# Optimization experiments

Hardware: AMD Instinct MI355X
Metric: run time of the kernel (lower is better)

## Reference

```python
import jax, jax.numpy as jnp
import numpy as np

# Standard SMPL kinematic tree (child -> parent); root's entry unused.
PARENTS = np.array([0, 0, 0, 0, 1, 2, 3, 4, 5, 6, 7, 8, 9, 9, 9, 12, 13, 14, 16, 17, 18, 19, 20, 21], dtype=np.int32)
N_JOINTS = 24


def _rodrigues(r):
    # r: [..., 3] axis-angle -> [..., 3, 3] rotation matrices.
    # Original adds N(0,1e-8) noise to avoid div-by-zero; we use a deterministic eps.
    theta = jnp.linalg.norm(r, axis=-1, keepdims=True) + 1e-8
    rh = r / theta
    cos = jnp.cos(theta)[..., None]
    sin = jnp.sin(theta)[..., None]
    z = jnp.zeros_like(rh[..., 0])
    K = jnp.stack([z, -rh[..., 2], rh[..., 1],
                   rh[..., 2], z, -rh[..., 0],
                   -rh[..., 1], rh[..., 0], z], axis=-1).reshape(r.shape[:-1] + (3, 3))
    outer = rh[..., :, None] * rh[..., None, :]
    eye = jnp.eye(3, dtype=r.dtype)
    return cos * eye + (1.0 - cos) * outer + sin * K


def setup_inputs() -> dict:
    key = jax.random.key(0)
    ks = jax.random.split(key, 7)
    N, V, J, B = 512, 6890, 24, 10
    beta = jax.random.normal(ks[0], (N, B), dtype=jnp.float32)
    pose = jax.random.normal(ks[1], (N, J * 3), dtype=jnp.float32)
    v_template = jax.random.normal(ks[2], (V, 3), dtype=jnp.float32)
    shapedirs = jax.random.normal(ks[3], (V, 3, B), dtype=jnp.float32) * 0.03
    posedirs = jax.random.normal(ks[4], (V, 3, (J - 1) * 9), dtype=jnp.float32) * 0.01
    J_regressor = jax.random.uniform(ks[5], (J, V), dtype=jnp.float32)
    J_regressor = J_regressor / jnp.sum(J_regressor, axis=1, keepdims=True)  # NonNegUnitSum(axis=1)
    weights = jax.random.uniform(ks[6], (V, J), dtype=jnp.float32)
    weights = weights / jnp.sum(weights, axis=1, keepdims=True)  # NonNegUnitSum(axis=1)
    return {"beta": beta, "pose": pose, "v_template": v_template, "shapedirs": shapedirs,
            "posedirs": posedirs, "J_regressor": J_regressor, "weights": weights}


def reference(beta, pose, v_template, shapedirs, posedirs, J_regressor, weights):
    N = beta.shape[0]
    dt = beta.dtype
    # Shape blendshapes: [N,V,3]
    v_shaped = jnp.einsum('nb,vcb->nvc', beta, shapedirs) + v_template
    # Joint locations: [N,J,3]
    J_loc = jnp.einsum('jv,nvc->njc', J_regressor, v_shaped)
    # Per-joint rotations: [N,24,3,3]
    R = _rodrigues(pose.reshape(N, N_JOINTS, 3))
    # Pose blendshapes
    lrotmin = (R[:, 1:] - jnp.eye(3, dtype=dt)).reshape(N, (N_JOINTS - 1) * 9)
    v_posed = v_shaped + jnp.einsum('np,vcp->nvc', lrotmin, posedirs)
    # Kinematic chain of 4x4 transforms
    bottom = jnp.broadcast_to(jnp.array([0.0, 0.0, 0.0, 1.0], dtype=dt), (N, 1, 4))

    def make_T(Rm, t):  # [N,3,3], [N,3] -> [N,4,4]
        return jnp.concatenate([jnp.concatenate([Rm, t[..., None]], axis=-1), bottom], axis=-2)

    G = [make_T(R[:, 0], J_loc[:, 0])]
    for i in range(1, N_JOINTS):
        p = int(PARENTS[i])
        G.append(jnp.matmul(G[p], make_T(R[:, i], J_loc[:, i] - J_loc[:, p])))
    G = jnp.stack(G, axis=1)  # [N,24,4,4]
    # Remove rest-pose joint translation: G[...,:,3] -= G @ [J,0]
    Jh = jnp.concatenate([J_loc, jnp.zeros_like(J_loc[..., :1])], axis=-1)  # [N,24,4]
    RJ = jnp.einsum('njab,njb->nja', G, Jh)
    G = G - jnp.pad(RJ[..., None], ((0, 0), (0, 0), (0, 0), (3, 0)))
    # Linear blend skinning: per-vertex blended transform [N,V,4,4]
    T = jnp.einsum('njab,vj->nvab', G, weights)
    vh = jnp.concatenate([v_posed, jnp.ones_like(v_posed[..., :1])], axis=-1)  # [N,V,4]
    v = jnp.einsum('nvab,nvb->nva', T, vh)
    return v[..., :3]
```

## Files before the change

### kernel.cpp

```cpp
#include <hip/hip_runtime.h>

#define V_CNT 6890
#define N_B 512
#define NP 207
#define KPAD 224
#define RTOT 20670
#define RPAD 20736
#define PREP_BLKS 2268
#define JS1_BLKS 192
#define W_BLKS 27
#define FUSE_X 108
#define FUSE_BLKS 864

typedef unsigned short ushort_t;
typedef __attribute__((ext_vector_type(4))) float f32x4;
typedef __attribute__((ext_vector_type(8))) short s16x8;
typedef __attribute__((ext_vector_type(4))) short s16x4;

#define O_PART 0u
#define O_G2   65536u
#define O_A    655360u
#define O_W    917504u
#define O_B    1441792u

__device__ __constant__ int PAR[24] = {0,0,0,0,1,2,3,4,5,6,7,8,9,9,9,12,13,14,16,17,18,19,20,21};
__device__ __constant__ int LVL[36] = {
    1, 2, 3,-1,   4, 5, 6,-1,   7, 8, 9,-1,
   10,11,12,13,  14,-1,-1,-1,  15,16,17,-1,
   18,19,-1,-1,  20,21,-1,-1,  22,23,-1,-1};

__device__ __forceinline__ ushort_t f2bf(float f) {
    union { float f; unsigned u; } x; x.f = f;
    unsigned u = x.u + 0x7fffu + ((x.u >> 16) & 1u);
    return (ushort_t)(u >> 16);
}
__device__ __forceinline__ float bf2f(ushort_t h) {
    union { unsigned u; float f; } x; x.u = ((unsigned)h) << 16;
    return x.f;
}

__global__ __launch_bounds__(256) void k_pre(const float* __restrict__ pdirs,
                                             const float* __restrict__ sdirs,
                                             const float* __restrict__ vtemp,
                                             const float* __restrict__ jreg,
                                             const float* __restrict__ wts,
                                             ushort_t* __restrict__ Bswz,
                                             float* __restrict__ part,
                                             ushort_t* __restrict__ Wp) {
    int b = blockIdx.x;
    int tid = threadIdx.x;
    if (b < PREP_BLKS) {
        int g = b * 256 + tid;
        int rtile = g / 448;
        int rem = g - rtile * 448;
        int kc = rem >> 6;
        int lane = rem & 63;
        int quad = lane >> 4, lm = lane & 15;
        int r = rtile * 16 + lm;
        int k0 = kc * 32 + quad * 8;
        s16x8 pk;
        if (r < RTOT) {
            const float* pr = pdirs + (size_t)r * NP;
            const float* sr = sdirs + (size_t)r * 10;
#pragma unroll
            for (int i = 0; i < 8; i++) {
                int k = k0 + i;
                float v = 0.f;
                if (k < NP) v = pr[k];
                else if (k < 217) v = sr[k - NP];
                pk[i] = (short)f2bf(v);
            }
        } else {
#pragma unroll
            for (int i = 0; i < 8; i++) pk[i] = 0;
        }
        *(s16x8*)(Bswz + (size_t)g * 8) = pk;
    } else if (b < PREP_BLKS + JS1_BLKS) {
        int b2 = b - PREP_BLKS;
        int ch = b2 & 7;
        int j = b2 >> 3;
        int v0 = ch * 862;
        int vend = v0 + 862; if (vend > V_CNT) vend = V_CNT;
        float acc[33];
#pragma unroll
        for (int i = 0; i < 33; i++) acc[i] = 0.f;
        for (int v = v0 + tid; v < vend; v += 256) {
            float r = jreg[j * V_CNT + v];
            const float* sd = sdirs + v * 30;
#pragma unroll
            for (int i = 0; i < 30; i++) acc[i] += r * sd[i];
            acc[30] += r * vtemp[v * 3 + 0];
            acc[31] += r * vtemp[v * 3 + 1];
            acc[32] += r * vtemp[v * 3 + 2];
        }
#pragma unroll
        for (int off = 32; off > 0; off >>= 1) {
#pragma unroll
            for (int i = 0; i < 33; i++) acc[i] += __shfl_down(acc[i], off);
        }
        __shared__ float red[4][33];
        int w = tid >> 6, lane = tid & 63;
        if (lane == 0) {
#pragma unroll
            for (int i = 0; i < 33; i++) red[w][i] = acc[i];
        }
        __syncthreads();
        if (tid < 33) {
            float s = red[0][tid] + red[1][tid] + red[2][tid] + red[3][tid];
            part[b2 * 33 + tid] = s;
        }
    } else {
        int v = (b - PREP_BLKS - JS1_BLKS) * 256 + tid;
        ushort_t o[32];
        if (v < V_CNT) {
            const float* wr = wts + v * 24;
#pragma unroll
            for (int j = 0; j < 24; j++) o[j] = f2bf(wr[j]);
        } else {
#pragma unroll
            for (int j = 0; j < 24; j++) o[j] = 0;
        }
#pragma unroll
        for (int j = 24; j < 32; j++) o[j] = 0;
#pragma unroll
        for (int q = 0; q < 4; q++)
            *(s16x8*)(Wp + (size_t)v * 32 + q * 8) = *(s16x8*)&o[q * 8];
    }
}

__global__ __launch_bounds__(128) void k_chain(const float* __restrict__ beta,
                                               const float* __restrict__ pose,
                                               const float* __restrict__ part,
                                               ushort_t* __restrict__ G2,
                                               ushort_t* __restrict__ Aswz) {
    __shared__ float JSl[720];
    __shared__ float JTl[72];
    __shared__ float Rl[2][24][9];
    __shared__ float Jl[2][24][3];
    __shared__ float Tm[2][24][16];
    __shared__ float G[2][24][16];
    __shared__ float Gp[2][24][12];
    int tid = threadIdx.x;

    for (int t = tid; t < 792; t += 128) {
        int j = t / 33, i = t - j * 33;
        float s = 0.f;
#pragma unroll
        for (int c = 0; c < 8; c++) s += part[(j * 8 + c) * 33 + i];
        if (i < 30) JSl[j * 30 + i] = s;
        else        JTl[j * 3 + (i - 30)] = s;
    }
    __syncthreads();

    int sub = tid >> 6, lane = tid & 63;
    int n = blockIdx.x * 2 + sub;

    if (lane < 24) {
        int t = lane;
        float x = pose[n * 72 + t * 3 + 0];
        float y = pose[n * 72 + t * 3 + 1];
        float z = pose[n * 72 + t * 3 + 2];
        float th = sqrtf(x * x + y * y + z * z) + 1e-8f;
        float inv = 1.f / th;
        float rx = x * inv, ry = y * inv, rz = z * inv;
        float c = cosf(th), s = sinf(th), omc = 1.f - c;
        Rl[sub][t][0] = c + omc * rx * rx;
        Rl[sub][t][1] = omc * rx * ry - s * rz;
        Rl[sub][t][2] = omc * rx * rz + s * ry;
        Rl[sub][t][3] = omc * ry * rx + s * rz;
        Rl[sub][t][4] = c + omc * ry * ry;
        Rl[sub][t][5] = omc * ry * rz - s * rx;
        Rl[sub][t][6] = omc * rz * rx - s * ry;
        Rl[sub][t][7] = omc * rz * ry + s * rx;
        Rl[sub][t][8] = c + omc * rz * rz;
#pragma unroll
        for (int cc = 0; cc < 3; cc++) {
            float a = JTl[t * 3 + cc];
#pragma unroll
            for (int b = 0; b < 10; b++) a += beta[n * 10 + b] * JSl[(t * 3 + cc) * 10 + b];
            Jl[sub][t][cc] = a;
        }
    }
    __syncthreads();
    if (lane < 24) {
        int t = lane;
        int p = PAR[t];
        float tx, ty, tz;
        if (t == 0) { tx = Jl[sub][0][0]; ty = Jl[sub][0][1]; tz = Jl[sub][0][2]; }
        else { tx = Jl[sub][t][0] - Jl[sub][p][0]; ty = Jl[sub][t][1] - Jl[sub][p][1]; tz = Jl[sub][t][2] - Jl[sub][p][2]; }
        Tm[sub][t][0] = Rl[sub][t][0]; Tm[sub][t][1] = Rl[sub][t][1]; Tm[sub][t][2]  = Rl[sub][t][2]; Tm[sub][t][3]  = tx;
        Tm[sub][t][4] = Rl[sub][t][3]; Tm[sub][t][5] = Rl[sub][t][4]; Tm[sub][t][6]  = Rl[sub][t][5]; Tm[sub][t][7]  = ty;
        Tm[sub][t][8] = Rl[sub][t][6]; Tm[sub][t][9] = Rl[sub][t][7]; Tm[sub][t][10] = Rl[sub][t][8]; Tm[sub][t][11] = tz;
        Tm[sub][t][12] = 0.f; Tm[sub][t][13] = 0.f; Tm[sub][t][14] = 0.f; Tm[sub][t][15] = 1.f;
    }
    __syncthreads();
    if (lane < 16) G[sub][0][lane] = Tm[sub][0][lane];
    __syncthreads();
#pragma unroll
    for (int p9 = 0; p9 < 9; p9++) {
        int slot = lane >> 4, el = lane & 15;
        int j = LVL[p9 * 4 + slot];
        if (j >= 0) {
            int par = PAR[j];
            int a = el >> 2, bb = el & 3;
            float s = G[sub][par][a * 4 + 0] * Tm[sub][j][0 * 4 + bb]
                    + G[sub][par][a * 4 + 1] * Tm[sub][j][1 * 4 + bb]
                    + G[sub][par][a * 4 + 2] * Tm[sub][j][2 * 4 + bb]
                    + G[sub][par][a * 4 + 3] * Tm[sub][j][3 * 4 + bb];
            G[sub][j][el] = s;
        }
        __syncthreads();
    }
    if (lane < 24) {
        int t = lane;
        float jx = Jl[sub][t][0], jy = Jl[sub][t][1], jz = Jl[sub][t][2];
#pragma unroll
        for (int a = 0; a < 3; a++) {
            float g0 = G[sub][t][a * 4 + 0], g1 = G[sub][t][a * 4 + 1];
            float g2 = G[sub][t][a * 4 + 2], g3 = G[sub][t][a * 4 + 3];
            Gp[sub][t][a * 4 + 0] = g0;
            Gp[sub][t][a * 4 + 1] = g1;
            Gp[sub][t][a * 4 + 2] = g2;
            Gp[sub][t][a * 4 + 3] = g3 - (g0 * jx + g1 * jy + g2 * jz);
        }
    }
    __syncthreads();
    {
        int quad = lane >> 4, lm = lane & 15;
        s16x8 pk;
#pragma unroll
        for (int jj = 0; jj < 8; jj++) {
            int joint = quad * 8 + jj;
            float val = (joint < 24 && lm < 12) ? Gp[sub][joint][lm] : 0.f;
            pk[jj] = (short)f2bf(val);
        }
        *(s16x8*)(G2 + (size_t)n * 512 + lane * 8) = pk;
    }
    if (lane < 28) {
        int kc = lane >> 2, quad2 = lane & 3;
        s16x8 pk;
#pragma unroll
        for (int j = 0; j < 8; j++) {
            int k = kc * 32 + quad2 * 8 + j;
            float val;
            if (k < NP) {
                int jo = 1 + k / 9;
                int e = k - (jo - 1) * 9;
                float d = (e == 0 || e == 4 || e == 8) ? 1.f : 0.f;
                val = Rl[sub][jo][e] - d;
            } else if (k < 217) {
                val = beta[n * 10 + (k - NP)];
            } else val = 0.f;
            pk[j] = (short)f2bf(val);
        }
        *(s16x8*)(Aswz + (((size_t)(n >> 4) * 7 + kc) * 64 + (quad2 * 16 + (n & 15))) * 8) = pk;
    }
}

__global__ __launch_bounds__(256) void k_fused(const ushort_t* __restrict__ Aswz,
                                               const ushort_t* __restrict__ Bswz,
                                               const ushort_t* __restrict__ Wp,
                                               const ushort_t* __restrict__ G2,
                                               const float* __restrict__ vtemp,
                                               float* __restrict__ out) {
    __shared__ ushort_t vp[4][96][36];
    int bid = blockIdx.x;
    int tt = (bid & 7) * FUSE_X + (bid >> 3);
    int bx = tt >> 3, by = tt & 7;
    int tid = threadIdx.x, w = tid >> 6, lane = tid & 63;
    int quad = lane >> 4, lm = lane & 15;
    int rh = w & 1, nh = w >> 1;
    int n_w = by * 64 + nh * 32;
    int vs_w = bx * 64 + rh * 32;
    int rtile0 = bx * 12 + rh * 6;
    int ntile0 = by * 4 + nh * 2;

    f32x4 acc[2][6];
#pragma unroll
    for (int a = 0; a < 2; a++)
#pragma unroll
        for (int b = 0; b < 6; b++) acc[a][b] = (f32x4)0.f;

    s16x8 af[2][2], bf[2][6];
#pragma unroll
    for (int mt = 0; mt < 2; mt++)
        af[0][mt] = *(const s16x8*)(Aswz + ((size_t)(ntile0 + mt) * 7 + 0) * 512 + lane * 8);
#pragma unroll
    for (int rt = 0; rt < 6; rt++)
        bf[0][rt] = *(const s16x8*)(Bswz + ((size_t)(rtile0 + rt) * 7 + 0) * 512 + lane * 8);
#pragma unroll
    for (int kc = 0; kc < 7; kc++) {
        int cur = kc & 1, nxt = cur ^ 1;
        if (kc < 6) {
#pragma unroll
            for (int mt = 0; mt < 2; mt++)
                af[nxt][mt] = *(const s16x8*)(Aswz + ((size_t)(ntile0 + mt) * 7 + kc + 1) * 512 + lane * 8);
#pragma unroll
            for (int rt = 0; rt < 6; rt++)
                bf[nxt][rt] = *(const s16x8*)(Bswz + ((size_t)(rtile0 + rt) * 7 + kc + 1) * 512 + lane * 8);
        }
#pragma unroll
        for (int mt = 0; mt < 2; mt++)
#pragma unroll
            for (int rt = 0; rt < 6; rt++)
                acc[mt][rt] = __builtin_amdgcn_mfma_f32_16x16x32_bf16(af[cur][mt], bf[cur][rt], acc[mt][rt], 0, 0, 0);
    }

    float vt[6];
#pragma unroll
    for (int rt = 0; rt < 6; rt++) {
        int col = bx * 192 + rh * 96 + rt * 16 + lm;
        vt[rt] = (col < RTOT) ? vtemp[col] : 0.f;
    }
#pragma unroll
    for (int mt = 0; mt < 2; mt++) {
#pragma unroll
        for (int rt = 0; rt < 6; rt++) {
            int rl = rt * 16 + lm;
            int nl0 = mt * 16 + quad * 4;
            s16x4 pk;
            pk[0] = (short)f2bf(acc[mt][rt][0] + vt[rt]);
            pk[1] = (short)f2bf(acc[mt][rt][1] + vt[rt]);
            pk[2] = (short)f2bf(acc[mt][rt][2] + vt[rt]);
            pk[3] = (short)f2bf(acc[mt][rt][3] + vt[rt]);
            *(s16x4*)&vp[w][rl][nl0] = pk;
        }
    }

    s16x8 wf[2];
#pragma unroll
    for (int mt = 0; mt < 2; mt++)
        wf[mt] = *(const s16x8*)(Wp + (size_t)(vs_w + mt * 16 + lm) * 32 + quad * 8);

    s16x8 ga = *(const s16x8*)(G2 + (size_t)n_w * 512 + lane * 8);
    s16x8 gb = *(const s16x8*)(G2 + (size_t)(n_w + 1) * 512 + lane * 8);
#pragma unroll 1
    for (int t = 0; t < 16; t++) {
        int na = n_w + 2 * t;
        s16x8 gan, gbn;
        if (t < 15) {
            gan = *(const s16x8*)(G2 + (size_t)(na + 2) * 512 + lane * 8);
            gbn = *(const s16x8*)(G2 + (size_t)(na + 3) * 512 + lane * 8);
        }
        f32x4 ta[2], tb[2];
#pragma unroll
        for (int mt = 0; mt < 2; mt++) {
            ta[mt] = __builtin_amdgcn_mfma_f32_16x16x32_bf16(ga, wf[mt], (f32x4)0.f, 0, 0, 0);
            tb[mt] = __builtin_amdgcn_mfma_f32_16x16x32_bf16(gb, wf[mt], (f32x4)0.f, 0, 0, 0);
        }
        if (quad < 3) {
#pragma unroll
            for (int mt = 0; mt < 2; mt++) {
                int v = vs_w + mt * 16 + lm;
                if (v < V_CNT) {
                    int vloc = mt * 16 + lm;
                    unsigned pw0 = *(const unsigned*)&vp[w][vloc * 3 + 0][2 * t];
                    unsigned pw1 = *(const unsigned*)&vp[w][vloc * 3 + 1][2 * t];
                    unsigned pw2 = *(const unsigned*)&vp[w][vloc * 3 + 2][2 * t];
                    float p0a = bf2f((ushort_t)(pw0 & 0xffffu)), p0b = bf2f((ushort_t)(pw0 >> 16));
                    float p1a = bf2f((ushort_t)(pw1 & 0xffffu)), p1b = bf2f((ushort_t)(pw1 >> 16));
                    float p2a = bf2f((ushort_t)(pw2 & 0xffffu)), p2b = bf2f((ushort_t)(pw2 >> 16));
                    float oa = ta[mt][3] + ta[mt][0] * p0a + ta[mt][1] * p1a + ta[mt][2] * p2a;
                    float ob = tb[mt][3] + tb[mt][0] * p0b + tb[mt][1] * p1b + tb[mt][2] * p2b;
                    out[((size_t)na * V_CNT + v) * 3 + quad] = oa;
                    out[((size_t)(na + 1) * V_CNT + v) * 3 + quad] = ob;
                }
            }
        }
        ga = gan; gb = gbn;
    }
}

extern "C" void kernel_launch(void* const* d_in, const int* in_sizes, int n_in,
                              void* d_out, int out_size, void* d_ws, size_t ws_size,
                              hipStream_t stream) {
    const float* beta  = (const float*)d_in[0];
    const float* pose  = (const float*)d_in[1];
    const float* vtemp = (const float*)d_in[2];
    const float* sdirs = (const float*)d_in[3];
    const float* pdirs = (const float*)d_in[4];
    const float* jreg  = (const float*)d_in[5];
    const float* wts   = (const float*)d_in[6];
    char* ws = (char*)d_ws;
    float*    ws_part = (float*)(ws + O_PART);
    ushort_t* ws_G2   = (ushort_t*)(ws + O_G2);
    ushort_t* ws_A    = (ushort_t*)(ws + O_A);
    ushort_t* ws_W    = (ushort_t*)(ws + O_W);
    ushort_t* ws_B    = (ushort_t*)(ws + O_B);
    float* out = (float*)d_out;

    k_pre<<<dim3(PREP_BLKS + JS1_BLKS + W_BLKS), dim3(256), 0, stream>>>(
        pdirs, sdirs, vtemp, jreg, wts, ws_B, ws_part, ws_W);
    k_chain<<<dim3(N_B / 2), dim3(128), 0, stream>>>(beta, pose, ws_part, ws_G2, ws_A);
    k_fused<<<dim3(FUSE_BLKS), dim3(256), 0, stream>>>(ws_A, ws_B, ws_W, ws_G2, vtemp, out);
}
```

Baseline: 137.8 us.

## Fuse posedirs and weights bf16 conversion into the main GEMM kernel

Drops the pre-pass that converted posedirs/shapedirs and skinning weights to swizzled bf16 workspace buffers. The fused kernel now reads fp32 posedirs and weights directly and converts them in registers before the MFMA. This removes a full write-then-read round trip of the large posedirs matrix (~17 MB fp32). The cost is that each posedirs element is re-read by every n-tile block, about eight times, in fp32 with unaligned, uncoalesced row-strided loads. The software double-buffering of the K loop is also lost.

```diff
diff --git a/kernel.cpp b/kernel.cpp
--- a/kernel.cpp
+++ b/kernel.cpp
@@ -3,12 +3,8 @@
 #define V_CNT 6890
 #define N_B 512
 #define NP 207
-#define KPAD 224
 #define RTOT 20670
-#define RPAD 20736
-#define PREP_BLKS 2268
 #define JS1_BLKS 192
-#define W_BLKS 27
 #define FUSE_X 108
 #define FUSE_BLKS 864
 
@@ -20,8 +16,6 @@
 #define O_PART 0u
 #define O_G2   65536u
 #define O_A    655360u
-#define O_W    917504u
-#define O_B    1441792u
 
 __device__ __constant__ int PAR[24] = {0,0,0,0,1,2,3,4,5,6,7,8,9,9,9,12,13,14,16,17,18,19,20,21};
 __device__ __constant__ int LVL[36] = {
@@ -38,93 +32,47 @@
     union { unsigned u; float f; } x; x.u = ((unsigned)h) << 16;
     return x.f;
 }
-
-__global__ __launch_bounds__(256) void k_pre(const float* __restrict__ pdirs,
+__device__ __forceinline__ f32x4 ld4u(const float* p) {
+    f32x4 v; __builtin_memcpy(&v, p, 16); return v;
+}
+
+__global__ __launch_bounds__(256) void k_pre(const float* __restrict__ jreg,
                                              const float* __restrict__ sdirs,
                                              const float* __restrict__ vtemp,
-                                             const float* __restrict__ jreg,
-                                             const float* __restrict__ wts,
-                                             ushort_t* __restrict__ Bswz,
-                                             float* __restrict__ part,
-                                             ushort_t* __restrict__ Wp) {
-    int b = blockIdx.x;
+                                             float* __restrict__ part) {
+    int b2 = blockIdx.x;
     int tid = threadIdx.x;
-    if (b < PREP_BLKS) {
-        int g = b * 256 + tid;
-        int rtile = g / 448;
-        int rem = g - rtile * 448;
-        int kc = rem >> 6;
-        int lane = rem & 63;
-        int quad = lane >> 4, lm = lane & 15;
-        int r = rtile * 16 + lm;
-        int k0 = kc * 32 + quad * 8;
-        s16x8 pk;
-        if (r < RTOT) {
-            const float* pr = pdirs + (size_t)r * NP;
-            const float* sr = sdirs + (size_t)r * 10;
-#pragma unroll
-            for (int i = 0; i < 8; i++) {
-                int k = k0 + i;
-                float v = 0.f;
-                if (k < NP) v = pr[k];
-                else if (k < 217) v = sr[k - NP];
-                pk[i] = (short)f2bf(v);
-            }
-        } else {
-#pragma unroll
-            for (int i = 0; i < 8; i++) pk[i] = 0;
-        }
-        *(s16x8*)(Bswz + (size_t)g * 8) = pk;
-    } else if (b < PREP_BLKS + JS1_BLKS) {
-        int b2 = b - PREP_BLKS;
-        int ch = b2 & 7;
-        int j = b2 >> 3;
-        int v0 = ch * 862;
-        int vend = v0 + 862; if (vend > V_CNT) vend = V_CNT;
-        float acc[33];
-#pragma unroll
-        for (int i = 0; i < 33; i++) acc[i] = 0.f;
-        for (int v = v0 + tid; v < vend; v += 256) {
-            float r = jreg[j * V_CNT + v];
-            const float* sd = sdirs + v * 30;
-#pragma unroll
-            for (int i = 0; i < 30; i++) acc[i] += r * sd[i];
-            acc[30] += r * vtemp[v * 3 + 0];
-            acc[31] += r * vtemp[v * 3 + 1];
-            acc[32] += r * vtemp[v * 3 + 2];
-        }
-#pragma unroll
-        for (int off = 32; off > 0; off >>= 1) {
-#pragma unroll
-            for (int i = 0; i < 33; i++) acc[i] += __shfl_down(acc[i], off);
-        }
-        __shared__ float red[4][33];
-        int w = tid >> 6, lane = tid & 63;
-        if (lane == 0) {
-#pragma unroll
-            for (int i = 0; i < 33; i++) red[w][i] = acc[i];
-        }
-        __syncthreads();
-        if (tid < 33) {
-            float s = red[0][tid] + red[1][tid] + red[2][tid] + red[3][tid];
-            part[b2 * 33 + tid] = s;
-        }
-    } else {
-        int v = (b - PREP_BLKS - JS1_BLKS) * 256 + tid;
-        ushort_t o[32];
-        if (v < V_CNT) {
-            const float* wr = wts + v * 24;
-#pragma unroll
-            for (int j = 0; j < 24; j++) o[j] = f2bf(wr[j]);
-        } else {
-#pragma unroll
-            for (int j = 0; j < 24; j++) o[j] = 0;
-        }
-#pragma unroll
-        for (int j = 24; j < 32; j++) o[j] = 0;
-#pragma unroll
-        for (int q = 0; q < 4; q++)
-            *(s16x8*)(Wp + (size_t)v * 32 + q * 8) = *(s16x8*)&o[q * 8];
+    int ch = b2 & 7;
+    int j = b2 >> 3;
+    int v0 = ch * 862;
+    int vend = v0 + 862; if (vend > V_CNT) vend = V_CNT;
+    float acc[33];
+#pragma unroll
+    for (int i = 0; i < 33; i++) acc[i] = 0.f;
+    for (int v = v0 + tid; v < vend; v += 256) {
+        float r = jreg[j * V_CNT + v];
+        const float* sd = sdirs + v * 30;
+#pragma unroll
+        for (int i = 0; i < 30; i++) acc[i] += r * sd[i];
+        acc[30] += r * vtemp[v * 3 + 0];
+        acc[31] += r * vtemp[v * 3 + 1];
+        acc[32] += r * vtemp[v * 3 + 2];
+    }
+#pragma unroll
+    for (int off = 32; off > 0; off >>= 1) {
+#pragma unroll
+        for (int i = 0; i < 33; i++) acc[i] += __shfl_down(acc[i], off);
+    }
+    __shared__ float red[4][33];
+    int w = tid >> 6, lane = tid & 63;
+    if (lane == 0) {
+#pragma unroll
+        for (int i = 0; i < 33; i++) red[w][i] = acc[i];
+    }
+    __syncthreads();
+    if (tid < 33) {
+        float s = red[0][tid] + red[1][tid] + red[2][tid] + red[3][tid];
+        part[b2 * 33 + tid] = s;
     }
 }
 
@@ -258,8 +206,9 @@
 }
 
 __global__ __launch_bounds__(256) void k_fused(const ushort_t* __restrict__ Aswz,
-                                               const ushort_t* __restrict__ Bswz,
-                                               const ushort_t* __restrict__ Wp,
+                                               const float* __restrict__ pdirs,
+                                               const float* __restrict__ sdirs,
+                                               const float* __restrict__ wts,
                                                const ushort_t* __restrict__ G2,
                                                const float* __restrict__ vtemp,
                                                float* __restrict__ out) {
@@ -275,35 +224,76 @@
     int rtile0 = bx * 12 + rh * 6;
     int ntile0 = by * 4 + nh * 2;
 
+    const float* prow[6];
+    bool rok[6];
+#pragma unroll
+    for (int rt = 0; rt < 6; rt++) {
+        int r = (rtile0 + rt) * 16 + lm;
+        rok[rt] = (r < RTOT);
+        int rs = rok[rt] ? r : 0;
+        prow[rt] = pdirs + (size_t)rs * NP;
+    }
+
     f32x4 acc[2][6];
 #pragma unroll
     for (int a = 0; a < 2; a++)
 #pragma unroll
         for (int b = 0; b < 6; b++) acc[a][b] = (f32x4)0.f;
 
-    s16x8 af[2][2], bf[2][6];
-#pragma unroll
-    for (int mt = 0; mt < 2; mt++)
-        af[0][mt] = *(const s16x8*)(Aswz + ((size_t)(ntile0 + mt) * 7 + 0) * 512 + lane * 8);
-#pragma unroll
-    for (int rt = 0; rt < 6; rt++)
-        bf[0][rt] = *(const s16x8*)(Bswz + ((size_t)(rtile0 + rt) * 7 + 0) * 512 + lane * 8);
-#pragma unroll
-    for (int kc = 0; kc < 7; kc++) {
-        int cur = kc & 1, nxt = cur ^ 1;
-        if (kc < 6) {
-#pragma unroll
-            for (int mt = 0; mt < 2; mt++)
-                af[nxt][mt] = *(const s16x8*)(Aswz + ((size_t)(ntile0 + mt) * 7 + kc + 1) * 512 + lane * 8);
+#pragma unroll 1
+    for (int kc = 0; kc < 6; kc++) {
+        s16x8 af[2], bfr[6];
+#pragma unroll
+        for (int mt = 0; mt < 2; mt++)
+            af[mt] = *(const s16x8*)(Aswz + ((size_t)(ntile0 + mt) * 7 + kc) * 512 + lane * 8);
+#pragma unroll
+        for (int rt = 0; rt < 6; rt++) {
+            s16x8 pk = (s16x8)0;
+            if (rok[rt]) {
+                const float* pr = prow[rt] + kc * 32 + quad * 8;
+                f32x4 x0 = ld4u(pr), x1 = ld4u(pr + 4);
+#pragma unroll
+                for (int i = 0; i < 4; i++) {
+                    pk[i]     = (short)f2bf(x0[i]);
+                    pk[i + 4] = (short)f2bf(x1[i]);
+                }
+            }
+            bfr[rt] = pk;
+        }
+#pragma unroll
+        for (int mt = 0; mt < 2; mt++)
 #pragma unroll
             for (int rt = 0; rt < 6; rt++)
-                bf[nxt][rt] = *(const s16x8*)(Bswz + ((size_t)(rtile0 + rt) * 7 + kc + 1) * 512 + lane * 8);
-        }
+                acc[mt][rt] = __builtin_amdgcn_mfma_f32_16x16x32_bf16(af[mt], bfr[rt], acc[mt][rt], 0, 0, 0);
+    }
+    {
+        s16x8 af[2], bfr[6];
 #pragma unroll
         for (int mt = 0; mt < 2; mt++)
+            af[mt] = *(const s16x8*)(Aswz + ((size_t)(ntile0 + mt) * 7 + 6) * 512 + lane * 8);
+#pragma unroll
+        for (int rt = 0; rt < 6; rt++) {
+            s16x8 pk = (s16x8)0;
+            if (rok[rt]) {
+                int r = (rtile0 + rt) * 16 + lm;
+                const float* pr = prow[rt];
+                const float* sr = sdirs + (size_t)r * 10;
+#pragma unroll
+                for (int i = 0; i < 8; i++) {
+                    int k = 192 + quad * 8 + i;
+                    float v = 0.f;
+                    if (k < NP) v = pr[k];
+                    else if (k < 217) v = sr[k - NP];
+                    pk[i] = (short)f2bf(v);
+                }
+            }
+            bfr[rt] = pk;
+        }
+#pragma unroll
+        for (int mt = 0; mt < 2; mt++)
 #pragma unroll
             for (int rt = 0; rt < 6; rt++)
-                acc[mt][rt] = __builtin_amdgcn_mfma_f32_16x16x32_bf16(af[cur][mt], bf[cur][rt], acc[mt][rt], 0, 0, 0);
+                acc[mt][rt] = __builtin_amdgcn_mfma_f32_16x16x32_bf16(af[mt], bfr[rt], acc[mt][rt], 0, 0, 0);
     }
 
     float vt[6];
@@ -329,8 +319,20 @@
 
     s16x8 wf[2];
 #pragma unroll
-    for (int mt = 0; mt < 2; mt++)
-        wf[mt] = *(const s16x8*)(Wp + (size_t)(vs_w + mt * 16 + lm) * 32 + quad * 8);
+    for (int mt = 0; mt < 2; mt++) {
+        int v = vs_w + mt * 16 + lm;
+        s16x8 pk = (s16x8)0;
+        if (quad < 3 && v < V_CNT) {
+            const float* wr = wts + (size_t)v * 24 + quad * 8;
+            f32x4 x0 = ld4u(wr), x1 = ld4u(wr + 4);
+#pragma unroll
+            for (int i = 0; i < 4; i++) {
+                pk[i]     = (short)f2bf(x0[i]);
+                pk[i + 4] = (short)f2bf(x1[i]);
+            }
+        }
+        wf[mt] = pk;
+    }
 
     s16x8 ga = *(const s16x8*)(G2 + (size_t)n_w * 512 + lane * 8);
     s16x8 gb = *(const s16x8*)(G2 + (size_t)(n_w + 1) * 512 + lane * 8);
@@ -385,12 +387,9 @@
     float*    ws_part = (float*)(ws + O_PART);
     ushort_t* ws_G2   = (ushort_t*)(ws + O_G2);
     ushort_t* ws_A    = (ushort_t*)(ws + O_A);
-    ushort_t* ws_W    = (ushort_t*)(ws + O_W);
-    ushort_t* ws_B    = (ushort_t*)(ws + O_B);
     float* out = (float*)d_out;
 
-    k_pre<<<dim3(PREP_BLKS + JS1_BLKS + W_BLKS), dim3(256), 0, stream>>>(
-        pdirs, sdirs, vtemp, jreg, wts, ws_B, ws_part, ws_W);
+    k_pre<<<dim3(JS1_BLKS), dim3(256), 0, stream>>>(jreg, sdirs, vtemp, ws_part);
     k_chain<<<dim3(N_B / 2), dim3(128), 0, stream>>>(beta, pose, ws_part, ws_G2, ws_A);
-    k_fused<<<dim3(FUSE_BLKS), dim3(256), 0, stream>>>(ws_A, ws_B, ws_W, ws_G2, vtemp, out);
-}
+    k_fused<<<dim3(FUSE_BLKS), dim3(256), 0, stream>>>(ws_A, pdirs, sdirs, wts, ws_G2, vtemp, out);
+}
```

Result: slower. 165.5 us (+20.1%).
